# Performance work log

Measured on AMD Instinct MI355X. Metric: run time of the kernel, lower is better.

The kernel has to match this reference:

```python
import jax, jax.numpy as jnp
import numpy as np

STEP = 0.01  # matches init kwarg step=0.01


def _disc(x, step=STEP):
    """Discretize like pd.cut with bins arange(floor(min), ceil(max)+step, step).
    Bin identity is all that matters for entropy, so we return integer bin ids.
    (Boundary convention: half-open floor binning; pd.cut uses right-closed,
    which differs only on exact bin edges - measure-zero for continuous data.)"""
    lower = jnp.floor(jnp.min(x))
    return jnp.floor((x - lower) / step).astype(jnp.int32)


def _row_joint_entropy(labels_list):
    """Per-row empirical (joint) entropy in nats of discrete label tuples.
    H_row = -sum_v p_v log p_v = -(1/n) * sum_i log(count(x_i)/n),
    computed via pairwise-equality counts (vectorized Counter).
    labels_list: list of [B, n] int arrays. Returns [B]."""
    eq = None
    for lab in labels_list:
        e = lab[:, :, None] == lab[:, None, :]  # [B, n, n]
        eq = e if eq is None else (eq & e)
    n = labels_list[0].shape[1]
    counts = eq.sum(-1).astype(jnp.float32)  # [B, n]
    return -jnp.mean(jnp.log(counts / n), axis=-1)  # [B]


def _h_soft(o, d):
    """F.cross_entropy(o, softmax(d), 'mean') - F.kl_div(log_softmax(o), softmax(d), 'mean').
    Note torch kl_div 'mean' averages over ALL elements (B*C)."""
    p = jax.nn.softmax(d, axis=-1)
    logq = jax.nn.log_softmax(o, axis=-1)
    ce = -jnp.mean(jnp.sum(p * logq, axis=-1))          # mean over batch
    kl = jnp.mean(p * (jnp.log(p) - logq))               # mean over B*C
    return ce - kl


def reference(data, data1, data2, data3, output1, output2, output3, output):
    # --- reconstruction term ---
    mse_loss = 0.5 * jnp.mean((data - output) ** 2)

    # --- discrete entropies on detached inputs (torch: .detach().numpy()) ---
    d1 = _disc(jax.lax.stop_gradient(data1))
    d2 = _disc(jax.lax.stop_gradient(data2))
    d3 = _disc(jax.lax.stop_gradient(data3))

    H_data_1 = jnp.mean(_row_joint_entropy([d1]))
    H_data_2 = jnp.mean(_row_joint_entropy([d2]))
    H_data_3 = jnp.mean(_row_joint_entropy([d3]))

    H_output_1 = _h_soft(output1, data1)
    H_output_2 = _h_soft(output2, data2)
    H_output_3 = _h_soft(output3, data3)

    H_1 = H_data_1 - H_output_1
    H_2 = H_data_2 - H_output_2
    H_3 = H_data_3 - H_output_3

    # equal widths -> pad_matrices is a no-op
    H_in_1_3 = jnp.mean(_row_joint_entropy([d1, d3]))
    H_in_2_3 = jnp.mean(_row_joint_entropy([d2, d3]))
    H_in_1_2 = jnp.mean(_row_joint_entropy([d1, d2]))

    in1_3 = jnp.concatenate((data1, data3), axis=1)
    in2_3 = jnp.concatenate((data2, data3), axis=1)
    in1_2 = jnp.concatenate((data1, data2), axis=1)
    out1_3 = jnp.concatenate((output1, output3), axis=1)
    out2_3 = jnp.concatenate((output2, output3), axis=1)
    out1_2 = jnp.concatenate((output1, output2), axis=1)

    H_out_1_3 = _h_soft(out1_3, in1_3)
    H_out_2_3 = _h_soft(out2_3, in2_3)
    H_out_1_2 = _h_soft(out1_2, in1_2)

    data1_3 = H_data_1 + H_data_3 - H_in_1_3
    data2_3 = H_data_2 + H_data_3 - H_in_2_3
    data1_2 = H_data_1 + H_data_2 - H_in_1_2
    label1_3 = H_output_1 + H_output_3 - H_out_1_3
    label2_3 = H_output_2 + H_output_3 - H_out_2_3
    label1_2 = H_output_1 + H_output_2 - H_out_1_2

    H_MI1_3 = label1_3 - data1_3
    H_MI2_3 = label2_3 - data2_3
    H_MI1_2 = label1_2 - data1_2

    # per-row conditional MI I(X1; X2 | X3) = H(X1,X3)+H(X2,X3)-H(X3)-H(X1,X2,X3),
    # summed over rows (torch loop accumulates cmi per row without averaging)
    cmi_rows = (_row_joint_entropy([d1, d3]) + _row_joint_entropy([d2, d3])
                - _row_joint_entropy([d3]) - _row_joint_entropy([d1, d2, d3]))
    ave_data_ConMI = jnp.sum(cmi_rows)

    in123 = jnp.concatenate((data1, data2, data3), axis=1)
    out123 = jnp.concatenate((output1, output2, output3), axis=1)
    H_output_123 = _h_soft(out123, in123)
    ave_label_ConMI = H_out_2_3 - H_output_3 + H_out_1_3 - H_output_123
    CMI = ave_label_ConMI - ave_data_ConMI

    return (0.5 * mse_loss
            + 0.25 * (jnp.square(H_1) + jnp.square(H_2) + jnp.square(H_3))
            + 0.25 * (jnp.square(H_MI1_3) + jnp.square(H_MI2_3)
                      + jnp.square(H_MI1_2) + jnp.square(CMI)))


def setup_inputs() -> dict:
    key = jax.random.key(0)
    ks = jax.random.split(key, 8)
    B, D, DT = 2048, 256, 768
    return {
        "data": jax.random.normal(ks[0], (B, DT), dtype=jnp.float32),
        "data1": jax.random.normal(ks[1], (B, D), dtype=jnp.float32),
        "data2": jax.random.normal(ks[2], (B, D), dtype=jnp.float32),
        "data3": jax.random.normal(ks[3], (B, D), dtype=jnp.float32),
        "output1": jax.random.normal(ks[4], (B, D), dtype=jnp.float32),
        "output2": jax.random.normal(ks[5], (B, D), dtype=jnp.float32),
        "output3": jax.random.normal(ks[6], (B, D), dtype=jnp.float32),
        "output": jax.random.normal(ks[7], (B, DT), dtype=jnp.float32),
    }
```

## Files before the change

### kernel.cpp

```cpp
#include <hip/hip_runtime.h>
#include <math.h>

#define B_ROWS 2048
#define NCOL   256
#define DTOT   768
#define HSLOTS 512
#define SBINS  1280

#define LO (-6.0f)


__device__ __forceinline__ int hslot0(unsigned key) {
    return (int)((key * 0x9E3779B1u) >> 23);
}

__device__ __forceinline__ int hfix(unsigned* __restrict__ h, int slot,
                                    unsigned key, unsigned prev) {
    while (true) {
        if (prev == 0u) return slot;
        if ((prev >> 10) == key) { atomicAdd(&h[slot], 1u); return slot; }
        slot = (slot + 1) & (HSLOTS - 1);
        prev = atomicCAS(&h[slot], 0u, (key << 10) + 1u);
    }
}

__global__ __launch_bounds__(64)
void row_kernel(const float* __restrict__ d1, const float* __restrict__ d2,
                const float* __restrict__ d3,
                const float* __restrict__ o1, const float* __restrict__ o2,
                const float* __restrict__ o3,
                const float* __restrict__ data, const float* __restrict__ outp,
                double* __restrict__ ws) {
    __shared__ unsigned lds[4 * HSLOTS + 3 * (SBINS / 2)];

    const int r = blockIdx.x, lane = threadIdx.x;

    const float4 X1 = ((const float4*)(d1 + r * NCOL))[lane];
    const float4 X2 = ((const float4*)(d2 + r * NCOL))[lane];
    const float4 X3 = ((const float4*)(d3 + r * NCOL))[lane];
    const float4 Y1 = ((const float4*)(o1 + r * NCOL))[lane];
    const float4 Y2 = ((const float4*)(o2 + r * NCOL))[lane];
    const float4 Y3 = ((const float4*)(o3 + r * NCOL))[lane];
    const float x1[4] = {X1.x, X1.y, X1.z, X1.w};
    const float x2[4] = {X2.x, X2.y, X2.z, X2.w};
    const float x3[4] = {X3.x, X3.y, X3.z, X3.w};
    const float y1[4] = {Y1.x, Y1.y, Y1.z, Y1.w};
    const float y2[4] = {Y2.x, Y2.y, Y2.z, Y2.w};
    const float y3[4] = {Y3.x, Y3.y, Y3.z, Y3.w};

    float ms = 0.f;
    #pragma unroll
    for (int t = 0; t < 3; ++t) {
        const float4 a = ((const float4*)(data + r * DTOT))[lane + 64 * t];
        const float4 o = ((const float4*)(outp + r * DTOT))[lane + 64 * t];
        const float dx = a.x - o.x, dy = a.y - o.y, dz = a.z - o.z, dw = a.w - o.w;
        ms += dx * dx + dy * dy + dz * dz + dw * dw;
    }

    {
        uint4* h4 = (uint4*)lds;
        for (int z = lane; z < (4 * HSLOTS + 3 * (SBINS / 2)) / 4; z += 64)
            h4[z] = make_uint4(0u, 0u, 0u, 0u);
    }
    __syncthreads();

    unsigned* t13  = lds;
    unsigned* t23  = lds + HSLOTS;
    unsigned* t12  = lds + 2 * HSLOTS;
    unsigned* t123 = lds + 3 * HSLOTS;
    unsigned* c1   = lds + 4 * HSLOTS;
    unsigned* c2   = c1 + SBINS / 2;
    unsigned* c3   = c2 + SBINS / 2;

    unsigned kk1[4], kk2[4], kk3[4];
    int SLa[4], SLb[4], SLc[4], SLd[4];
    float sv[12] = {0,0,0,0,0,0,0,0,0,0,0,0};
    #pragma unroll
    for (int j = 0; j < 4; ++j) {
        const unsigned k1 = (unsigned)(int)floorf((x1[j] - LO) / 0.01f);
        const unsigned k2 = (unsigned)(int)floorf((x2[j] - LO) / 0.01f);
        const unsigned k3 = (unsigned)(int)floorf((x3[j] - LO) / 0.01f);
        kk1[j] = k1; kk2[j] = k2; kk3[j] = k3;
        atomicAdd(&c1[k1 >> 1], 1u << ((k1 & 1u) * 16u));
        atomicAdd(&c2[k2 >> 1], 1u << ((k2 & 1u) * 16u));
        atomicAdd(&c3[k3 >> 1], 1u << ((k3 & 1u) * 16u));
        const unsigned k13 = k1 | (k3 << 11), k23 = k2 | (k3 << 11), k12 = k1 | (k2 << 11);
        int s13 = hslot0(k13), s23 = hslot0(k23), s12 = hslot0(k12);
        const unsigned p13 = atomicCAS(&t13[s13], 0u, (k13 << 10) + 1u);
        const unsigned p23 = atomicCAS(&t23[s23], 0u, (k23 << 10) + 1u);
        const unsigned p12 = atomicCAS(&t12[s12], 0u, (k12 << 10) + 1u);
        s13 = hfix(t13, s13, k13, p13);
        SLa[j] = s13;
        SLb[j] = hfix(t23, s23, k23, p23);
        SLc[j] = hfix(t12, s12, k12, p12);
        const unsigned k123 = (unsigned)s13 | (k2 << 9);
        int s123 = hslot0(k123);
        const unsigned p123 = atomicCAS(&t123[s123], 0u, (k123 << 10) + 1u);
        SLd[j] = hfix(t123, s123, k123, p123);

        const float ed1 = __expf(x1[j]), ed2 = __expf(x2[j]), ed3 = __expf(x3[j]);
        sv[0] += ed1; sv[1] += ed1 * y1[j]; sv[2]  += ed1 * x1[j]; sv[3]  += __expf(y1[j]);
        sv[4] += ed2; sv[5] += ed2 * y2[j]; sv[6]  += ed2 * x2[j]; sv[7]  += __expf(y2[j]);
        sv[8] += ed3; sv[9] += ed3 * y3[j]; sv[10] += ed3 * x3[j]; sv[11] += __expf(y3[j]);
    }

    float logacc[7] = {0,0,0,0,0,0,0};
    #pragma unroll
    for (int j = 0; j < 4; ++j) {
        const unsigned w1 = c1[kk1[j] >> 1], w2 = c2[kk2[j] >> 1], w3 = c3[kk3[j] >> 1];
        logacc[0] += __logf((float)((w1 >> ((kk1[j] & 1u) * 16u)) & 0xFFFFu));
        logacc[1] += __logf((float)((w2 >> ((kk2[j] & 1u) * 16u)) & 0xFFFFu));
        logacc[2] += __logf((float)((w3 >> ((kk3[j] & 1u) * 16u)) & 0xFFFFu));
        logacc[3] += __logf((float)(t13[SLa[j]]  & 1023u));
        logacc[4] += __logf((float)(t23[SLb[j]]  & 1023u));
        logacc[5] += __logf((float)(t12[SLc[j]]  & 1023u));
        logacc[6] += __logf((float)(t123[SLd[j]] & 1023u));
    }

    float svt[12];
    #pragma unroll
    for (int s = 0; s < 12; ++s) {
        float x = sv[s];
        for (int off = 32; off; off >>= 1) x += __shfl_xor(x, off);
        svt[s] = x;
    }
    float lgt[7];
    #pragma unroll
    for (int s = 0; s < 7; ++s) {
        float x = logacc[s];
        for (int off = 32; off; off >>= 1) x += __shfl_xor(x, off);
        lgt[s] = x;
    }
    float mst = ms;
    for (int off = 32; off; off >>= 1) mst += __shfl_xor(mst, off);

    float fin = mst;
    if (lane < 7) {
        #pragma unroll
        for (int s = 0; s < 7; ++s) fin = (lane == s) ? lgt[s] : fin;
    } else if (lane < 21) {
        const int mi = (lane < 14) ? lane - 7 : lane - 14;
        const int M[7] = {1, 2, 4, 5, 6, 3, 7};
        int mk = 0;
        #pragma unroll
        for (int s = 0; s < 7; ++s) mk = (mi == s) ? M[s] : mk;
        float Zd = 0.f, Td = 0.f, Ud = 0.f, Zo = 0.f;
        #pragma unroll
        for (int k = 0; k < 3; ++k) {
            const float c = (float)((mk >> k) & 1);
            Zd += c * svt[4*k]; Td += c * svt[4*k+1];
            Ud += c * svt[4*k+2]; Zo += c * svt[4*k+3];
        }
        const float Ld = __logf(Zd), Lo = __logf(Zo);
        const float Spo = Td / Zd, Spd = Ud / Zd;
        fin = (lane < 14) ? (Lo - Spo) : ((Spd - Ld) - (Spo - Lo));
    }
    if (lane < 22) ws[lane * B_ROWS + r] = (double)fin;
}

__global__ __launch_bounds__(1024)
void fold_kernel(const double* __restrict__ ws, float* __restrict__ out) {
    __shared__ double T[22];
    const int tid = threadIdx.x, w = tid >> 6, lane = tid & 63;
    for (int s = w; s < 22; s += 16) {
        double acc = 0.0;
        #pragma unroll
        for (int i = 0; i < 32; ++i) acc += ws[s * B_ROWS + lane + 64 * i];
        for (int off = 32; off; off >>= 1) acc += __shfl_xor(acc, off);
        if (lane == 0) T[s] = acc;
    }
    __syncthreads();
    if (tid == 0) {
        const double n = 256.0, Bd = 2048.0;
        const double logn = log(n);
        const double S1 = T[0], S2 = T[1], S3 = T[2];
        const double S13 = T[3], S23 = T[4], S12 = T[5], S123 = T[6];
        const double Hd1   = logn - S1  / (Bd * n);
        const double Hd2   = logn - S2  / (Bd * n);
        const double Hd3   = logn - S3  / (Bd * n);
        const double Hin13 = logn - S13 / (Bd * n);
        const double Hin23 = logn - S23 / (Bd * n);
        const double Hin12 = logn - S12 / (Bd * n);
        const double C[7] = {256, 256, 256, 512, 512, 512, 768};
        double Ho[7];
        for (int m = 0; m < 7; ++m) Ho[m] = T[7 + m] / Bd - T[14 + m] / (Bd * C[m]);
        const double H1 = Hd1 - Ho[0], H2 = Hd2 - Ho[1], H3 = Hd3 - Ho[2];
        const double MI13 = (Ho[0] + Ho[2] - Ho[3]) - (Hd1 + Hd3 - Hin13);
        const double MI23 = (Ho[1] + Ho[2] - Ho[4]) - (Hd2 + Hd3 - Hin23);
        const double MI12 = (Ho[0] + Ho[1] - Ho[5]) - (Hd1 + Hd2 - Hin12);
        const double aveD = -(S13 + S23 - S3 - S123) / n;
        const double aveL = Ho[4] - Ho[2] + Ho[3] - Ho[6];
        const double CMI = aveL - aveD;
        const double mse = 0.5 * T[21] / (Bd * 768.0);
        out[0] = (float)(0.5 * mse
                       + 0.25 * (H1 * H1 + H2 * H2 + H3 * H3)
                       + 0.25 * (MI13 * MI13 + MI23 * MI23 + MI12 * MI12
                                 + CMI * CMI));
    }
}

extern "C" void kernel_launch(void* const* d_in, const int* in_sizes, int n_in,
                              void* d_out, int out_size, void* d_ws, size_t ws_size,
                              hipStream_t stream) {
    const float* data = (const float*)d_in[0];
    const float* d1   = (const float*)d_in[1];
    const float* d2   = (const float*)d_in[2];
    const float* d3   = (const float*)d_in[3];
    const float* o1   = (const float*)d_in[4];
    const float* o2   = (const float*)d_in[5];
    const float* o3   = (const float*)d_in[6];
    const float* outp = (const float*)d_in[7];

    double* ws = (double*)d_ws;

    row_kernel<<<B_ROWS, 64, 0, stream>>>(d1, d2, d3, o1, o2, o3, data, outp, ws);
    fold_kernel<<<1, 1024, 0, stream>>>(ws, (float*)d_out);
}
```

Baseline: 106.9 us.

## Use DPP wave reductions, banked double atomics, and restructure LDS zeroing

Replaces shuffle-based wave reductions with DPP row operations plus a readlane, and accumulates per-row partials into 16 banks of double atomics instead of writing a full per-row workspace. The fold kernel then sums only 16 entries per quantity. LDS zeroing moves before the global loads so it can overlap with them, and the LDS array is rounded up to 4096 words. This adds a zeroing kernel launch and relies on double atomicAdd contention and non-deterministic summation order.

```diff
diff --git a/kernel.cpp b/kernel.cpp
--- a/kernel.cpp
+++ b/kernel.cpp
@@ -4,11 +4,17 @@
 #define B_ROWS 2048
 #define NCOL   256
 #define DTOT   768
+#define BANKS  16
 #define HSLOTS 512
 #define SBINS  1280
 
+
 #define LO (-6.0f)
 
+__global__ __launch_bounds__(256)
+void zero_kernel(double* __restrict__ acc) {
+    for (int z = threadIdx.x; z < BANKS * 22; z += 256) acc[z] = 0.0;
+}
 
 __device__ __forceinline__ int hslot0(unsigned key) {
     return (int)((key * 0x9E3779B1u) >> 23);
@@ -24,16 +30,36 @@
     }
 }
 
+#define DPP_ADD(x, ctrl, rm, bm)                                               \
+    x += __int_as_float(__builtin_amdgcn_update_dpp(                           \
+        0, __float_as_int(x), ctrl, rm, bm, false))
+
+__device__ __forceinline__ float wsum(float x) {
+    DPP_ADD(x, 0x111, 0xf, 0xf);
+    DPP_ADD(x, 0x112, 0xf, 0xf);
+    DPP_ADD(x, 0x114, 0xf, 0xe);
+    DPP_ADD(x, 0x118, 0xf, 0xc);
+    DPP_ADD(x, 0x142, 0xa, 0xf);
+    DPP_ADD(x, 0x143, 0xc, 0xf);
+    return __int_as_float(__builtin_amdgcn_readlane(__float_as_int(x), 63));
+}
+
 __global__ __launch_bounds__(64)
 void row_kernel(const float* __restrict__ d1, const float* __restrict__ d2,
                 const float* __restrict__ d3,
                 const float* __restrict__ o1, const float* __restrict__ o2,
                 const float* __restrict__ o3,
                 const float* __restrict__ data, const float* __restrict__ outp,
-                double* __restrict__ ws) {
-    __shared__ unsigned lds[4 * HSLOTS + 3 * (SBINS / 2)];
+                double* __restrict__ acc) {
+    __shared__ unsigned lds[4096];
 
     const int r = blockIdx.x, lane = threadIdx.x;
+
+    {
+        uint4* h4 = (uint4*)lds;
+        #pragma unroll
+        for (int z = 0; z < 16; ++z) h4[lane + z * 64] = make_uint4(0u, 0u, 0u, 0u);
+    }
 
     const float4 X1 = ((const float4*)(d1 + r * NCOL))[lane];
     const float4 X2 = ((const float4*)(d2 + r * NCOL))[lane];
@@ -55,12 +81,6 @@
         const float4 o = ((const float4*)(outp + r * DTOT))[lane + 64 * t];
         const float dx = a.x - o.x, dy = a.y - o.y, dz = a.z - o.z, dw = a.w - o.w;
         ms += dx * dx + dy * dy + dz * dz + dw * dw;
-    }
-
-    {
-        uint4* h4 = (uint4*)lds;
-        for (int z = lane; z < (4 * HSLOTS + 3 * (SBINS / 2)) / 4; z += 64)
-            h4[z] = make_uint4(0u, 0u, 0u, 0u);
     }
     __syncthreads();
 
@@ -119,20 +139,11 @@
 
     float svt[12];
     #pragma unroll
-    for (int s = 0; s < 12; ++s) {
-        float x = sv[s];
-        for (int off = 32; off; off >>= 1) x += __shfl_xor(x, off);
-        svt[s] = x;
-    }
+    for (int s = 0; s < 12; ++s) svt[s] = wsum(sv[s]);
     float lgt[7];
     #pragma unroll
-    for (int s = 0; s < 7; ++s) {
-        float x = logacc[s];
-        for (int off = 32; off; off >>= 1) x += __shfl_xor(x, off);
-        lgt[s] = x;
-    }
-    float mst = ms;
-    for (int off = 32; off; off >>= 1) mst += __shfl_xor(mst, off);
+    for (int s = 0; s < 7; ++s) lgt[s] = wsum(logacc[s]);
+    const float mst = wsum(ms);
 
     float fin = mst;
     if (lane < 7) {
@@ -155,22 +166,21 @@
         const float Spo = Td / Zd, Spd = Ud / Zd;
         fin = (lane < 14) ? (Lo - Spo) : ((Spd - Ld) - (Spo - Lo));
     }
-    if (lane < 22) ws[lane * B_ROWS + r] = (double)fin;
-}
-
-__global__ __launch_bounds__(1024)
-void fold_kernel(const double* __restrict__ ws, float* __restrict__ out) {
+    if (lane < 22) atomicAdd(&acc[(r & (BANKS - 1)) * 22 + lane], (double)fin);
+}
+
+__global__ __launch_bounds__(64)
+void fold_kernel(const double* __restrict__ acc, float* __restrict__ out) {
     __shared__ double T[22];
-    const int tid = threadIdx.x, w = tid >> 6, lane = tid & 63;
-    for (int s = w; s < 22; s += 16) {
-        double acc = 0.0;
-        #pragma unroll
-        for (int i = 0; i < 32; ++i) acc += ws[s * B_ROWS + lane + 64 * i];
-        for (int off = 32; off; off >>= 1) acc += __shfl_xor(acc, off);
-        if (lane == 0) T[s] = acc;
+    const int lane = threadIdx.x;
+    if (lane < 22) {
+        double s = 0.0;
+        #pragma unroll
+        for (int bk = 0; bk < BANKS; ++bk) s += acc[bk * 22 + lane];
+        T[lane] = s;
     }
     __syncthreads();
-    if (tid == 0) {
+    if (lane == 0) {
         const double n = 256.0, Bd = 2048.0;
         const double logn = log(n);
         const double S1 = T[0], S2 = T[1], S3 = T[2];
@@ -211,8 +221,9 @@
     const float* o3   = (const float*)d_in[6];
     const float* outp = (const float*)d_in[7];
 
-    double* ws = (double*)d_ws;
-
-    row_kernel<<<B_ROWS, 64, 0, stream>>>(d1, d2, d3, o1, o2, o3, data, outp, ws);
-    fold_kernel<<<1, 1024, 0, stream>>>(ws, (float*)d_out);
-}
+    double* acc = (double*)d_ws;
+
+    zero_kernel<<<1, 256, 0, stream>>>(acc);
+    row_kernel<<<B_ROWS, 64, 0, stream>>>(d1, d2, d3, o1, o2, o3, data, outp, acc);
+    fold_kernel<<<1, 64, 0, stream>>>(acc, (float*)d_out);
+}
```

After: 102.9 us. -3.7%, faster.
